# Kernel tuning notes

Measured on AMD Instinct MI355X. Metric: run time of the kernel, lower is better.

Reference implementation:

```python
import jax, jax.numpy as jnp
from jax import lax
import numpy as np

NUM_CLASSES = 6
WIN = 11


def setup_inputs() -> dict:
    key = jax.random.key(0)
    k1, k2 = jax.random.split(key)
    x = jax.random.normal(k1, (8, NUM_CLASSES, 512, 512), dtype=jnp.float32)
    target = jax.random.randint(k2, (8, 1, 512, 512), 0, NUM_CLASSES, dtype=jnp.int32)
    return {"x": x, "target": target}


def reference(x, target):
    # log-softmax over class dim
    log_p = jax.nn.log_softmax(x, axis=1)  # [B,C,H,W]

    w = -jnp.ones((1, 1, WIN, WIN), dtype=jnp.float32)
    w = w.at[0, 0, WIN // 2, WIN // 2].set(float(WIN * WIN - 1))
    t = target.astype(jnp.float32)  # [B,1,H,W]
    edge = lax.conv_general_dilated(
        t, w, window_strides=(1, 1), padding='SAME',
        dimension_numbers=('NCHW', 'OIHW', 'NCHW'))
    edge_mask = (edge != 0).astype(jnp.float32)  # [B,1,H,W], binarized

    # dynamic smoothing = fraction of edge pixels, capped at 0.2
    s = jnp.minimum(jnp.mean(edge_mask), jnp.float32(0.2))

    labels = target[:, 0]  # [B,H,W]
    onehot = jax.nn.one_hot(labels, NUM_CLASSES, axis=1, dtype=jnp.float32)  # [B,C,H,W]
    # to_categorical(alpha=s): alpha off-class, 1 - alpha + alpha/C on-class
    soft = s * (1.0 - onehot) + (1.0 - s + s / NUM_CLASSES) * onehot

    mask = onehot * (1.0 - edge_mask) + soft * edge_mask  # [B,C,H,W]
    loss = jnp.mean(jnp.sum(mask * log_p, axis=1))
    return -loss
```

## Files before the change

### kernel.cpp

```cpp
#include <hip/hip_runtime.h>

#define BATCH   8
#define NCLS    6
#define HW      512
#define IMGPIX  (HW * HW)
#define NPIX    (BATCH * IMGPIX)
#define TILE    32
#define HALO    5
#define SM      (TILE + 2 * HALO)
#define RSTRIDE 36
#define NB      (BATCH * 256)

__device__ __forceinline__ float get4(const float4& v, int j) {
    return j == 0 ? v.x : j == 1 ? v.y : j == 2 ? v.z : v.w;
}

__global__ __launch_bounds__(256, 4) void ls_main_kernel(
        const float* __restrict__ x,
        const int*   __restrict__ tgt,
        float*       __restrict__ part) {
    __shared__ int   s_t[SM * SM];
    __shared__ int   s_rs[SM][RSTRIDE];
    __shared__ float sw1[4], sw2[4];
    __shared__ int   swe[4];

    const int tid  = threadIdx.x;
    const int blk  = blockIdx.x;
    const int b    = blk & 7;
    const int tile = blk >> 3;
    const int tr   = (tile >> 4) * TILE;
    const int tc   = (tile & 15) * TILE;

    const int* timg = tgt + b * IMGPIX;

    int tv[7];
#pragma unroll
    for (int i = 0; i < 7; i++) {
        const int e  = tid + i * 256;
        const int ly = e / SM;
        const int lx = e - ly * SM;
        int v = 0;
        if (e < SM * SM) {
            const int gy = tr - HALO + ly, gx = tc - HALO + lx;
            if (gy >= 0 && gy < HW && gx >= 0 && gx < HW) v = timg[gy * HW + gx];
        }
        tv[i] = v;
    }

    const int py = tid >> 3;
    const int px = (tid & 7) << 2;
    const int gy = tr + py;
    const int gx = tc + px;
    const float* xb = x + ((size_t)(b * NCLS) << 18) + (gy << 9) + gx;
    float4 xc[NCLS];
#pragma unroll
    for (int c = 0; c < NCLS; c++)
        xc[c] = *(const float4*)(xb + ((size_t)c << 18));

#pragma unroll
    for (int i = 0; i < 7; i++) {
        const int e = tid + i * 256;
        if (e < SM * SM) s_t[e] = tv[i];
    }
    __syncthreads();

    if (tid < SM * 4) {
        const int row  = tid >> 2;
        const int c0   = (tid & 3) << 3;
        const int base = row * SM + c0;
        int buf[18];
#pragma unroll
        for (int k = 0; k < 18; k++) buf[k] = s_t[base + k];
        int acc = 0;
#pragma unroll
        for (int k = 0; k < 11; k++) acc += buf[k];
        s_rs[row][c0] = acc;
#pragma unroll
        for (int k = 1; k < 8; k++) {
            acc += buf[k + 10] - buf[k - 1];
            s_rs[row][c0 + k] = acc;
        }
    }
    __syncthreads();

    int4 bs = make_int4(0, 0, 0, 0);
#pragma unroll
    for (int dy = 0; dy <= 2 * HALO; dy++) {
        const int4 r = *(const int4*)&s_rs[py + dy][px];
        bs.x += r.x; bs.y += r.y; bs.z += r.z; bs.w += r.w;
    }
    const int bsa[4] = {bs.x, bs.y, bs.z, bs.w};
    int t4[4];
#pragma unroll
    for (int j = 0; j < 4; j++) t4[j] = s_t[(py + HALO) * SM + px + HALO + j];

    float r1 = 0.f, r2 = 0.f;
    int ec = 0;
#pragma unroll
    for (int j = 0; j < 4; j++) {
        const float a0 = get4(xc[0], j), a1 = get4(xc[1], j), a2 = get4(xc[2], j);
        const float a3 = get4(xc[3], j), a4 = get4(xc[4], j), a5 = get4(xc[5], j);
        const float se = __expf(a0) + __expf(a1) + __expf(a2) +
                         __expf(a3) + __expf(a4) + __expf(a5);
        const float lse = __logf(se);
        const int   t   = t4[j];
        const float xt  = t == 0 ? a0 : t == 1 ? a1 : t == 2 ? a2 :
                          t == 3 ? a3 : t == 4 ? a4 : a5;
        const float lpl = xt - lse;
        r1 += lpl;
        const int ev = 121 * t - bsa[j];
        const int eb = (ev != 0) ? 1 : 0;
        const float S = (a0 + a1 + a2 + a3 + a4 + a5) - 6.f * lse;
        r2 = fmaf((float)eb, S - (11.0f / 6.0f) * lpl, r2);
        ec += eb;
    }

#pragma unroll
    for (int off = 32; off > 0; off >>= 1) {
        r1 += __shfl_down(r1, off);
        r2 += __shfl_down(r2, off);
        ec += __shfl_down(ec, off);
    }
    const int wave = tid >> 6;
    if ((tid & 63) == 0) { sw1[wave] = r1; sw2[wave] = r2; swe[wave] = ec; }
    __syncthreads();
    if (tid == 0) {
        part[blk]          = sw1[0] + sw1[1] + sw1[2] + sw1[3];
        part[NB + blk]     = sw2[0] + sw2[1] + sw2[2] + sw2[3];
        part[2 * NB + blk] = (float)(swe[0] + swe[1] + swe[2] + swe[3]);
    }
}

__global__ __launch_bounds__(256) void ls_finalize_kernel(
        const float* __restrict__ part,
        float* __restrict__ out) {
    const int tid = threadIdx.x;
    double d1 = 0.0, d2 = 0.0, de = 0.0;
#pragma unroll
    for (int i = 0; i < NB / 256; i++) {
        const int idx = tid + i * 256;
        d1 += (double)part[idx];
        d2 += (double)part[NB + idx];
        de += (double)part[2 * NB + idx];
    }
#pragma unroll
    for (int off = 32; off > 0; off >>= 1) {
        d1 += __shfl_down(d1, off);
        d2 += __shfl_down(d2, off);
        de += __shfl_down(de, off);
    }
    __shared__ double sd1[4], sd2[4], sde[4];
    const int wave = tid >> 6;
    if ((tid & 63) == 0) { sd1[wave] = d1; sd2[wave] = d2; sde[wave] = de; }
    __syncthreads();
    if (tid == 0) {
        const double R1 = sd1[0] + sd1[1] + sd1[2] + sd1[3];
        const double R2 = sd2[0] + sd2[1] + sd2[2] + sd2[3];
        const double E  = sde[0] + sde[1] + sde[2] + sde[3];
        const float  s  = fminf((float)E * (1.0f / (float)NPIX), 0.2f);
        const double loss = (R1 + (double)s * R2) * (1.0 / (double)NPIX);
        out[0] = (float)(-loss);
    }
}

extern "C" void kernel_launch(void* const* d_in, const int* in_sizes, int n_in,
                              void* d_out, int out_size, void* d_ws, size_t ws_size,
                              hipStream_t stream) {
    const float* x   = (const float*)d_in[0];
    const int*   tgt = (const int*)d_in[1];
    float*       out = (float*)d_out;
    float*       part = (float*)d_ws;

    ls_main_kernel<<<NB, 256, 0, stream>>>(x, tgt, part);
    ls_finalize_kernel<<<1, 256, 0, stream>>>(part, out);
}
```

Before: 89.45 us.

## Fuse finalize into main kernel via last-block counter and drop target smem staging

```diff
diff --git a/kernel.cpp b/kernel.cpp
--- a/kernel.cpp
+++ b/kernel.cpp
@@ -18,11 +18,13 @@
 __global__ __launch_bounds__(256, 4) void ls_main_kernel(
         const float* __restrict__ x,
         const int*   __restrict__ tgt,
-        float*       __restrict__ part) {
-    __shared__ int   s_t[SM * SM];
+        float*       __restrict__ part,
+        unsigned int* __restrict__ counter,
+        float*       __restrict__ out) {
     __shared__ int   s_rs[SM][RSTRIDE];
     __shared__ float sw1[4], sw2[4];
     __shared__ int   swe[4];
+    __shared__ bool  islast;
 
     const int tid  = threadIdx.x;
     const int blk  = blockIdx.x;
@@ -33,52 +35,41 @@
 
     const int* timg = tgt + b * IMGPIX;
 
-    int tv[7];
+    int buf[18];
+    const int hrow = tid >> 2;
+    const int hc0  = (tid & 3) << 3;
+    if (tid < SM * 4) {
+        const int  gyh = tr - HALO + hrow;
+        const bool vr  = (gyh >= 0 && gyh < HW);
+        const int* rp  = timg + gyh * HW;
+        const int  gx0 = tc + hc0 - HALO;
 #pragma unroll
-    for (int i = 0; i < 7; i++) {
-        const int e  = tid + i * 256;
-        const int ly = e / SM;
-        const int lx = e - ly * SM;
-        int v = 0;
-        if (e < SM * SM) {
-            const int gy = tr - HALO + ly, gx = tc - HALO + lx;
-            if (gy >= 0 && gy < HW && gx >= 0 && gx < HW) v = timg[gy * HW + gx];
+        for (int k = 0; k < 18; k++) {
+            const int gxk = gx0 + k;
+            buf[k] = (vr && gxk >= 0 && gxk < HW) ? rp[gxk] : 0;
         }
-        tv[i] = v;
     }
 
     const int py = tid >> 3;
     const int px = (tid & 7) << 2;
     const int gy = tr + py;
     const int gx = tc + px;
+    const int4 tq = *(const int4*)(timg + (gy << 9) + gx);
     const float* xb = x + ((size_t)(b * NCLS) << 18) + (gy << 9) + gx;
     float4 xc[NCLS];
 #pragma unroll
     for (int c = 0; c < NCLS; c++)
         xc[c] = *(const float4*)(xb + ((size_t)c << 18));
 
-#pragma unroll
-    for (int i = 0; i < 7; i++) {
-        const int e = tid + i * 256;
-        if (e < SM * SM) s_t[e] = tv[i];
-    }
-    __syncthreads();
-
     if (tid < SM * 4) {
-        const int row  = tid >> 2;
-        const int c0   = (tid & 3) << 3;
-        const int base = row * SM + c0;
-        int buf[18];
-#pragma unroll
-        for (int k = 0; k < 18; k++) buf[k] = s_t[base + k];
         int acc = 0;
 #pragma unroll
         for (int k = 0; k < 11; k++) acc += buf[k];
-        s_rs[row][c0] = acc;
+        s_rs[hrow][hc0] = acc;
 #pragma unroll
         for (int k = 1; k < 8; k++) {
             acc += buf[k + 10] - buf[k - 1];
-            s_rs[row][c0 + k] = acc;
+            s_rs[hrow][hc0 + k] = acc;
         }
     }
     __syncthreads();
@@ -90,9 +81,7 @@
         bs.x += r.x; bs.y += r.y; bs.z += r.z; bs.w += r.w;
     }
     const int bsa[4] = {bs.x, bs.y, bs.z, bs.w};
-    int t4[4];
-#pragma unroll
-    for (int j = 0; j < 4; j++) t4[j] = s_t[(py + HALO) * SM + px + HALO + j];
+    const int t4a[4] = {tq.x, tq.y, tq.z, tq.w};
 
     float r1 = 0.f, r2 = 0.f;
     int ec = 0;
@@ -103,7 +92,7 @@
         const float se = __expf(a0) + __expf(a1) + __expf(a2) +
                          __expf(a3) + __expf(a4) + __expf(a5);
         const float lse = __logf(se);
-        const int   t   = t4[j];
+        const int   t   = t4a[j];
         const float xt  = t == 0 ? a0 : t == 1 ? a1 : t == 2 ? a2 :
                           t == 3 ? a3 : t == 4 ? a4 : a5;
         const float lpl = xt - lse;
@@ -124,42 +113,46 @@
     const int wave = tid >> 6;
     if ((tid & 63) == 0) { sw1[wave] = r1; sw2[wave] = r2; swe[wave] = ec; }
     __syncthreads();
+
     if (tid == 0) {
-        part[blk]          = sw1[0] + sw1[1] + sw1[2] + sw1[3];
-        part[NB + blk]     = sw2[0] + sw2[1] + sw2[2] + sw2[3];
-        part[2 * NB + blk] = (float)(swe[0] + swe[1] + swe[2] + swe[3]);
+        const float R1 = sw1[0] + sw1[1] + sw1[2] + sw1[3];
+        const float R2 = sw2[0] + sw2[1] + sw2[2] + sw2[3];
+        const int   E  = swe[0] + swe[1] + swe[2] + swe[3];
+        __hip_atomic_store(&part[blk],          R1,       __ATOMIC_RELAXED, __HIP_MEMORY_SCOPE_AGENT);
+        __hip_atomic_store(&part[NB + blk],     R2,       __ATOMIC_RELAXED, __HIP_MEMORY_SCOPE_AGENT);
+        __hip_atomic_store(&part[2 * NB + blk], (float)E, __ATOMIC_RELAXED, __HIP_MEMORY_SCOPE_AGENT);
+        const unsigned prev = __hip_atomic_fetch_add(counter, 1u,
+                                  __ATOMIC_ACQ_REL, __HIP_MEMORY_SCOPE_AGENT);
+        islast = (prev == NB - 1);
     }
-}
+    __syncthreads();
 
-__global__ __launch_bounds__(256) void ls_finalize_kernel(
-        const float* __restrict__ part,
-        float* __restrict__ out) {
-    const int tid = threadIdx.x;
-    double d1 = 0.0, d2 = 0.0, de = 0.0;
+    if (islast) {
+        double d1 = 0.0, d2 = 0.0, de = 0.0;
 #pragma unroll
-    for (int i = 0; i < NB / 256; i++) {
-        const int idx = tid + i * 256;
-        d1 += (double)part[idx];
-        d2 += (double)part[NB + idx];
-        de += (double)part[2 * NB + idx];
-    }
+        for (int i = 0; i < NB / 256; i++) {
+            const int idx = tid + i * 256;
+            d1 += (double)__hip_atomic_load(&part[idx],          __ATOMIC_RELAXED, __HIP_MEMORY_SCOPE_AGENT);
+            d2 += (double)__hip_atomic_load(&part[NB + idx],     __ATOMIC_RELAXED, __HIP_MEMORY_SCOPE_AGENT);
+            de += (double)__hip_atomic_load(&part[2 * NB + idx], __ATOMIC_RELAXED, __HIP_MEMORY_SCOPE_AGENT);
+        }
 #pragma unroll
-    for (int off = 32; off > 0; off >>= 1) {
-        d1 += __shfl_down(d1, off);
-        d2 += __shfl_down(d2, off);
-        de += __shfl_down(de, off);
-    }
-    __shared__ double sd1[4], sd2[4], sde[4];
-    const int wave = tid >> 6;
-    if ((tid & 63) == 0) { sd1[wave] = d1; sd2[wave] = d2; sde[wave] = de; }
-    __syncthreads();
-    if (tid == 0) {
-        const double R1 = sd1[0] + sd1[1] + sd1[2] + sd1[3];
-        const double R2 = sd2[0] + sd2[1] + sd2[2] + sd2[3];
-        const double E  = sde[0] + sde[1] + sde[2] + sde[3];
-        const float  s  = fminf((float)E * (1.0f / (float)NPIX), 0.2f);
-        const double loss = (R1 + (double)s * R2) * (1.0 / (double)NPIX);
-        out[0] = (float)(-loss);
+        for (int off = 32; off > 0; off >>= 1) {
+            d1 += __shfl_down(d1, off);
+            d2 += __shfl_down(d2, off);
+            de += __shfl_down(de, off);
+        }
+        __shared__ double sd1[4], sd2[4], sde[4];
+        if ((tid & 63) == 0) { sd1[wave] = d1; sd2[wave] = d2; sde[wave] = de; }
+        __syncthreads();
+        if (tid == 0) {
+            const double R1 = sd1[0] + sd1[1] + sd1[2] + sd1[3];
+            const double R2 = sd2[0] + sd2[1] + sd2[2] + sd2[3];
+            const double E  = sde[0] + sde[1] + sde[2] + sde[3];
+            const float  s  = fminf((float)E * (1.0f / (float)NPIX), 0.2f);
+            const double loss = (R1 + (double)s * R2) * (1.0 / (double)NPIX);
+            out[0] = (float)(-loss);
+        }
     }
 }
 
@@ -169,8 +162,10 @@
     const float* x   = (const float*)d_in[0];
     const int*   tgt = (const int*)d_in[1];
     float*       out = (float*)d_out;
-    float*       part = (float*)d_ws;
 
-    ls_main_kernel<<<NB, 256, 0, stream>>>(x, tgt, part);
-    ls_finalize_kernel<<<1, 256, 0, stream>>>(part, out);
+    float*        part    = (float*)d_ws;
+    unsigned int* counter = (unsigned int*)((char*)d_ws + 3 * NB * 4);
+
+    hipMemsetAsync(counter, 0, 4, stream);
+    ls_main_kernel<<<NB, 256, 0, stream>>>(x, tgt, part, counter, out);
 }
```

Result: slower. 179.6 us (+100.8%).
